# Kernel optimization log

Measured on AMD Instinct MI355X. Metric: run time of the kernel, lower is better.

The kernel has to match this reference:

```python
import jax, jax.numpy as jnp
import numpy as np

PI = 3.14159265358979323846
MARGIN = 6.0
DIM = 256
ENT_TOT = 43234
REL_RANGE = (6.0 + 2.0) / DIM  # (margin + epsilon) / dim = 0.03125


def setup_inputs() -> dict:
    key = jax.random.key(0)
    k1, k2, k3 = jax.random.split(key, 3)
    head = jax.random.normal(k1, (32, 2 * DIM), dtype=jnp.float32)
    relation = jax.random.normal(k2, (32, DIM), dtype=jnp.float32)
    ent_emb = jax.random.normal(k3, (ENT_TOT, 2 * DIM), dtype=jnp.float32)
    return {"head": head, "relation": relation, "ent_emb": ent_emb}


def reference(head, relation, ent_emb):
    # head: (B, 2D) -> re/im halves (B, D)
    re_h, im_h = jnp.split(head, 2, axis=-1)
    # entity table: (E, 2D) -> (E, D) each
    re_t, im_t = jnp.split(ent_emb, 2, axis=-1)
    # phase rotation from relation embedding
    phase = relation / (REL_RANGE / PI)          # (B, D)
    re_r = jnp.cos(phase)
    im_r = jnp.sin(phase)
    # complex rotation of head by relation: (B, D)
    re_rot = re_h * re_r - im_h * im_r
    im_rot = re_h * im_r + im_h * re_r
    # difference against every entity, broadcast to (B, E, D)
    re_s = re_rot[:, None, :] - re_t[None, :, :]
    im_s = im_rot[:, None, :] - im_t[None, :, :]
    # L2 norm over the complex pair, summed over D -> (B, E)
    dist = jnp.sqrt(re_s * re_s + im_s * im_s).sum(axis=-1)
    return MARGIN - dist
```

## Files before the change

kernel.cpp:

```cpp
#include <hip/hip_runtime.h>
#include <math.h>

#define DIMH 256
#define NB   32
#define E_TOT 43234
#define TE   128
#define DK   32
#define DQ   64
#define PHASE_DIV 0.009947183943243459f

typedef float v2f __attribute__((ext_vector_type(2)));
typedef float v4f __attribute__((ext_vector_type(4)));

__global__ __launch_bounds__(256) void init_kernel(float* __restrict__ out) {
    int i = blockIdx.x * 256 + threadIdx.x;
    if (i < (NB * E_TOT) / 4) {
        float4 v = make_float4(6.0f, 6.0f, 6.0f, 6.0f);
        reinterpret_cast<float4*>(out)[i] = v;
    }
}

__global__ void rot_kernel(const float* __restrict__ head,
                           const float* __restrict__ rel,
                           float* __restrict__ rot) {
    int i = blockIdx.x * blockDim.x + threadIdx.x;
    int b = i >> 8;
    int d = i & 255;
    float re_h = head[b * 2 * DIMH + d];
    float im_h = head[b * 2 * DIMH + DIMH + d];
    float ph = rel[b * DIMH + d] / PHASE_DIV;
    float s, c;
    sincosf(ph, &s, &c);
    rot[b * DIMH + d]             = re_h * c - im_h * s;
    rot[NB * DIMH + b * DIMH + d] = re_h * s + im_h * c;
}

__device__ __forceinline__ v2f sqrt2(v2f s) {
    v2f r;
    r.x = __builtin_amdgcn_sqrtf(s.x);
    r.y = __builtin_amdgcn_sqrtf(s.y);
    return r;
}

__global__ __launch_bounds__(256, 3) void dist_kernel(const float* __restrict__ ent,
                                                      const float* __restrict__ rot,
                                                      float* __restrict__ out) {
    __shared__ v4f s_e[TE][DK / 2 + 1];
    __shared__ v4f s_r[NB][DK / 2 + 1];

    const int tid   = threadIdx.x;
    const int etile = blockIdx.x >> 2;
    const int quart = blockIdx.x & 3;
    const int eb    = etile * TE;
    const int eg    = tid & 31;
    const int bg    = (tid >> 5) * 4;
    const int dbase = quart * DQ;

    v2f acc[4][4];
    #pragma unroll
    for (int j = 0; j < 4; ++j)
        #pragma unroll
        for (int k = 0; k < 4; ++k) { acc[j][k].x = 0.f; acc[j][k].y = 0.f; }

    for (int c = 0; c < DQ / DK; ++c) {
        const int dk = dbase + c * DK;
        #pragma unroll
        for (int it = 0; it < 4; ++it) {
            int q   = tid + it * 256;
            int row = q >> 3;
            int c4  = q & 7;
            int er  = eb + row;
            if (er >= E_TOT) er = E_TOT - 1;
            const float* base = &ent[(size_t)er * (2 * DIMH)];
            float4 vre = *reinterpret_cast<const float4*>(base + dk + 4 * c4);
            float4 vim = *reinterpret_cast<const float4*>(base + DIMH + dk + 4 * c4);
            v4f lo, hi;
            lo.x = vre.x; lo.y = vre.y; lo.z = vim.x; lo.w = vim.y;
            hi.x = vre.z; hi.y = vre.w; hi.z = vim.z; hi.w = vim.w;
            s_e[row][2 * c4]     = lo;
            s_e[row][2 * c4 + 1] = hi;
        }
        {
            int row = tid >> 3;
            int c4  = tid & 7;
            float4 vrr = *reinterpret_cast<const float4*>(&rot[row * DIMH + dk + 4 * c4]);
            float4 vri = *reinterpret_cast<const float4*>(&rot[NB * DIMH + row * DIMH + dk + 4 * c4]);
            v4f lo, hi;
            lo.x = vrr.x; lo.y = vrr.y; lo.z = vri.x; lo.w = vri.y;
            hi.x = vrr.z; hi.y = vrr.w; hi.z = vri.z; hi.w = vri.w;
            s_r[row][2 * c4]     = lo;
            s_r[row][2 * c4 + 1] = hi;
        }
        __syncthreads();

        #pragma unroll 4
        for (int p = 0; p < DK / 2; ++p) {
            v4f r4[4], e4[4];
            #pragma unroll
            for (int j = 0; j < 4; ++j) r4[j] = s_r[bg + j][p];
            #pragma unroll
            for (int k = 0; k < 4; ++k) e4[k] = s_e[eg + 32 * k][p];
            #pragma unroll
            for (int j = 0; j < 4; ++j)
                #pragma unroll
                for (int k = 0; k < 4; ++k) {
                    v2f a = r4[j].xy - e4[k].xy;
                    v2f b = r4[j].zw - e4[k].zw;
                    v2f s = a * a + b * b;
                    acc[j][k] += sqrt2(s);
                }
        }
        __syncthreads();
    }

    #pragma unroll
    for (int k = 0; k < 4; ++k) {
        int e = eb + eg + 32 * k;
        if (e < E_TOT) {
            #pragma unroll
            for (int j = 0; j < 4; ++j)
                atomicAdd(&out[(size_t)(bg + j) * E_TOT + e],
                          -(acc[j][k].x + acc[j][k].y));
        }
    }
}

extern "C" void kernel_launch(void* const* d_in, const int* in_sizes, int n_in,
                              void* d_out, int out_size, void* d_ws, size_t ws_size,
                              hipStream_t stream) {
    const float* head = (const float*)d_in[0];
    const float* rel  = (const float*)d_in[1];
    const float* ent  = (const float*)d_in[2];
    float* rot = (float*)d_ws;

    int init_blocks = ((NB * E_TOT) / 4 + 255) / 256;
    init_kernel<<<init_blocks, 256, 0, stream>>>((float*)d_out);
    rot_kernel<<<(NB * DIMH) / 256, 256, 0, stream>>>(head, rel, rot);

    int etiles = (E_TOT + TE - 1) / TE;
    dist_kernel<<<etiles * 4, 256, 0, stream>>>(ent, rot, (float*)d_out);
}
```

Baseline: 178.6 us.

## Halve entity tile, split D in halves, and register-prefetch next chunk

Entity tiles shrink from 128 to 64 and the feature dimension is split across two blocks instead of four, so each block handles a 128-wide slice in four 32-wide chunks. Global loads for the next chunk are issued into registers right after the barrier, so they overlap with the sqrt/accumulate loop on the current chunk. Per-thread accumulators drop from 16 to 8 pairs and launch bounds rise to 6 blocks per CU for higher occupancy. The trade-off is that each block reuses each rotation row across fewer entities, and the prefetch holds extra registers live.

Result: slower. 209.7 us (+17.4%).

```diff
diff --git a/kernel.cpp b/kernel.cpp
--- a/kernel.cpp
+++ b/kernel.cpp
@@ -4,9 +4,10 @@
 #define DIMH 256
 #define NB   32
 #define E_TOT 43234
-#define TE   128
+#define TE   64
 #define DK   32
-#define DQ   64
+#define DQ   128
+#define NC   (DQ / DK)
 #define PHASE_DIV 0.009947183943243459f
 
 typedef float v2f __attribute__((ext_vector_type(2)));
@@ -42,68 +43,79 @@
     return r;
 }
 
-__global__ __launch_bounds__(256, 3) void dist_kernel(const float* __restrict__ ent,
+__global__ __launch_bounds__(256, 6) void dist_kernel(const float* __restrict__ ent,
                                                       const float* __restrict__ rot,
                                                       float* __restrict__ out) {
     __shared__ v4f s_e[TE][DK / 2 + 1];
     __shared__ v4f s_r[NB][DK / 2 + 1];
 
     const int tid   = threadIdx.x;
-    const int etile = blockIdx.x >> 2;
-    const int quart = blockIdx.x & 3;
+    const int etile = blockIdx.x >> 1;
+    const int half  = blockIdx.x & 1;
     const int eb    = etile * TE;
     const int eg    = tid & 31;
     const int bg    = (tid >> 5) * 4;
-    const int dbase = quart * DQ;
+    const int dbase = half * DQ;
 
-    v2f acc[4][4];
+    const int er0 = min(eb + (tid >> 3), E_TOT - 1);
+    const int er1 = min(eb + ((tid + 256) >> 3), E_TOT - 1);
+    const int ec0 = (tid & 7) << 2;
+    const int rrow = tid >> 3;
+
+    float4 pe_re[2], pe_im[2], p_rr, p_ri;
+
+    auto load_chunk = [&](int dk) {
+        const float* b0 = &ent[(size_t)er0 * (2 * DIMH)];
+        const float* b1 = &ent[(size_t)er1 * (2 * DIMH)];
+        pe_re[0] = *reinterpret_cast<const float4*>(b0 + dk + ec0);
+        pe_im[0] = *reinterpret_cast<const float4*>(b0 + DIMH + dk + ec0);
+        pe_re[1] = *reinterpret_cast<const float4*>(b1 + dk + ec0);
+        pe_im[1] = *reinterpret_cast<const float4*>(b1 + DIMH + dk + ec0);
+        p_rr = *reinterpret_cast<const float4*>(&rot[rrow * DIMH + dk + ec0]);
+        p_ri = *reinterpret_cast<const float4*>(&rot[NB * DIMH + rrow * DIMH + dk + ec0]);
+    };
+
+    v2f acc[4][2];
     #pragma unroll
     for (int j = 0; j < 4; ++j)
         #pragma unroll
-        for (int k = 0; k < 4; ++k) { acc[j][k].x = 0.f; acc[j][k].y = 0.f; }
+        for (int k = 0; k < 2; ++k) { acc[j][k].x = 0.f; acc[j][k].y = 0.f; }
 
-    for (int c = 0; c < DQ / DK; ++c) {
-        const int dk = dbase + c * DK;
-        #pragma unroll
-        for (int it = 0; it < 4; ++it) {
-            int q   = tid + it * 256;
-            int row = q >> 3;
-            int c4  = q & 7;
-            int er  = eb + row;
-            if (er >= E_TOT) er = E_TOT - 1;
-            const float* base = &ent[(size_t)er * (2 * DIMH)];
-            float4 vre = *reinterpret_cast<const float4*>(base + dk + 4 * c4);
-            float4 vim = *reinterpret_cast<const float4*>(base + DIMH + dk + 4 * c4);
+    load_chunk(dbase);
+
+    for (int c = 0; c < NC; ++c) {
+        {
+            int c4 = tid & 7;
+            #pragma unroll
+            for (int it = 0; it < 2; ++it) {
+                int row = (tid + it * 256) >> 3;
+                v4f lo, hi;
+                lo.x = pe_re[it].x; lo.y = pe_re[it].y; lo.z = pe_im[it].x; lo.w = pe_im[it].y;
+                hi.x = pe_re[it].z; hi.y = pe_re[it].w; hi.z = pe_im[it].z; hi.w = pe_im[it].w;
+                s_e[row][2 * c4]     = lo;
+                s_e[row][2 * c4 + 1] = hi;
+            }
             v4f lo, hi;
-            lo.x = vre.x; lo.y = vre.y; lo.z = vim.x; lo.w = vim.y;
-            hi.x = vre.z; hi.y = vre.w; hi.z = vim.z; hi.w = vim.w;
-            s_e[row][2 * c4]     = lo;
-            s_e[row][2 * c4 + 1] = hi;
-        }
-        {
-            int row = tid >> 3;
-            int c4  = tid & 7;
-            float4 vrr = *reinterpret_cast<const float4*>(&rot[row * DIMH + dk + 4 * c4]);
-            float4 vri = *reinterpret_cast<const float4*>(&rot[NB * DIMH + row * DIMH + dk + 4 * c4]);
-            v4f lo, hi;
-            lo.x = vrr.x; lo.y = vrr.y; lo.z = vri.x; lo.w = vri.y;
-            hi.x = vrr.z; hi.y = vrr.w; hi.z = vri.z; hi.w = vri.w;
-            s_r[row][2 * c4]     = lo;
-            s_r[row][2 * c4 + 1] = hi;
+            lo.x = p_rr.x; lo.y = p_rr.y; lo.z = p_ri.x; lo.w = p_ri.y;
+            hi.x = p_rr.z; hi.y = p_rr.w; hi.z = p_ri.z; hi.w = p_ri.w;
+            s_r[rrow][2 * c4]     = lo;
+            s_r[rrow][2 * c4 + 1] = hi;
         }
         __syncthreads();
 
+        if (c + 1 < NC) load_chunk(dbase + (c + 1) * DK);
+
         #pragma unroll 4
         for (int p = 0; p < DK / 2; ++p) {
-            v4f r4[4], e4[4];
+            v4f r4[4], e4[2];
             #pragma unroll
             for (int j = 0; j < 4; ++j) r4[j] = s_r[bg + j][p];
             #pragma unroll
-            for (int k = 0; k < 4; ++k) e4[k] = s_e[eg + 32 * k][p];
+            for (int k = 0; k < 2; ++k) e4[k] = s_e[eg + 32 * k][p];
             #pragma unroll
             for (int j = 0; j < 4; ++j)
                 #pragma unroll
-                for (int k = 0; k < 4; ++k) {
+                for (int k = 0; k < 2; ++k) {
                     v2f a = r4[j].xy - e4[k].xy;
                     v2f b = r4[j].zw - e4[k].zw;
                     v2f s = a * a + b * b;
@@ -114,7 +126,7 @@
     }
 
     #pragma unroll
-    for (int k = 0; k < 4; ++k) {
+    for (int k = 0; k < 2; ++k) {
         int e = eb + eg + 32 * k;
         if (e < E_TOT) {
             #pragma unroll
@@ -138,5 +150,5 @@
     rot_kernel<<<(NB * DIMH) / 256, 256, 0, stream>>>(head, rel, rot);
 
     int etiles = (E_TOT + TE - 1) / TE;
-    dist_kernel<<<etiles * 4, 256, 0, stream>>>(ent, rot, (float*)d_out);
+    dist_kernel<<<etiles * 2, 256, 0, stream>>>(ent, rot, (float*)d_out);
 }
```
